# Kernel tuning notes

Hardware: AMD Instinct MI355X
Metric: run time of the kernel (lower is better)

The kernel has to match this reference:

```python
import jax, jax.numpy as jnp
import numpy as np

SIN, TEMB, EMB, S = 128, 512, 1024, 64
BATCH, T = 4, 4096


def setup_inputs() -> dict:
    key = jax.random.key(0)
    ks = jax.random.split(key, 16)

    def w(k, *shape):
        return jax.random.normal(k, shape, jnp.float32) / np.float32(np.sqrt(shape[0]))

    return {
        "time_embed": jax.random.normal(ks[0], (SIN,), jnp.float32),
        "x": jax.random.normal(ks[1], (BATCH, T, EMB), jnp.float32),
        "W1": w(ks[2], SIN, TEMB), "b1": jnp.zeros((TEMB,), jnp.float32),
        "W2": w(ks[3], TEMB, TEMB), "b2": jnp.zeros((TEMB,), jnp.float32),
        "WA": w(ks[4], TEMB, S), "bA": jnp.zeros((S,), jnp.float32),
        "WB": w(ks[5], TEMB, S, EMB), "bB": jnp.zeros((S, EMB), jnp.float32),
        "WC": w(ks[6], TEMB, EMB, S), "bC": jnp.zeros((EMB, S), jnp.float32),
        "WD": w(ks[7], TEMB, EMB), "bD": jnp.zeros((EMB,), jnp.float32),
        "Wdl": w(ks[8], TEMB, S), "bdl": jnp.zeros((S,), jnp.float32),
        "MA": w(ks[9], SIN, S), "mA": jnp.zeros((S,), jnp.float32),
        "MB": w(ks[10], SIN, S, EMB), "mB": jnp.zeros((S, EMB), jnp.float32),
        "MC": w(ks[11], SIN, EMB, S), "mC": jnp.zeros((EMB, S), jnp.float32),
        "MD": w(ks[12], SIN, EMB), "mD": jnp.zeros((EMB,), jnp.float32),
        "Mdl": w(ks[13], SIN, S), "mdl": jnp.zeros((S,), jnp.float32),
    }


def _ssm_forward(time_embed, x, W1, b1, W2, b2, WA, bA, WB, bB, WC, bC, WD, bD,
                 Wdl, bdl, MA, mA, MB, mB, MC, mC, MD, mD, Mdl, mdl):
    # time-dependent parameter generation
    t = jax.nn.silu(time_embed @ W1 + b1)
    t = t @ W2 + b2  # [TEMB]

    A_base = -jax.nn.softplus(t @ WA + bA)                       # [S]
    B_base = jnp.einsum('t,tse->se', t, WB) + bB                 # [S,E]
    C_base = jnp.einsum('t,tes->es', t, WC) + bC                 # [E,S]
    D_base = t @ WD + bD                                         # [E]
    delta_base = jax.nn.softplus(t @ Wdl + bdl) + 1e-4           # [S]

    A = A_base * jax.nn.sigmoid(time_embed @ MA + mA)
    Bm = B_base * jax.nn.sigmoid(jnp.einsum('t,tse->se', time_embed, MB) + mB)
    C = C_base * jax.nn.sigmoid(jnp.einsum('t,tes->es', time_embed, MC) + mC)
    D = D_base * jax.nn.sigmoid(time_embed @ MD + mD)
    delta = delta_base * jax.nn.sigmoid(time_embed @ Mdl + mdl)  # [S]

    A_bar = jnp.exp(delta * A)          # [S]
    B_bar = delta[:, None] * Bm         # [S,E]

    xt = jnp.swapaxes(x, 0, 1)          # [T,B,E]

    def step(h, x_t):                   # h: [B,S], x_t: [B,E]
        h_new = A_bar * h + x_t @ B_bar.T
        y = h_new @ C.T                 # [B,E]
        return h_new, y

    h0 = jnp.zeros((x.shape[0], A_bar.shape[0]), x.dtype)
    _, ys = jax.lax.scan(step, h0, xt)  # ys: [T,B,E]
    return jnp.swapaxes(ys, 0, 1) + D * x


def reference(time_embed, x, W1, b1, W2, b2, WA, bA, WB, bB, WC, bC, WD, bD,
              Wdl, bdl, MA, mA, MB, mB, MC, mC, MD, mD, Mdl, mdl):
    return _ssm_forward(time_embed, x, W1, b1, W2, b2, WA, bA, WB, bB, WC, bC,
                        WD, bD, Wdl, bdl, MA, mA, MB, mB, MC, mC, MD, mD, Mdl, mdl)
```

## Files before the change

kernel.cpp:

```cpp
#include <hip/hip_runtime.h>
#include <math.h>

#define SIN_ 128
#define TEMB_ 512
#define EMB_ 1024
#define S_ 64
#define B_ 4
#define T_ 4096
#define NROW (B_*T_)
#define L_ 32
#define NC_ (T_/L_)

#define GK 32
#define NSL 16
#define NCH 16
#define NGCH 4

#define WS_T1     0
#define WS_T2     512
#define WS_DELTA  1024
#define WS_ABAR   1088
#define WS_EL     1152
#define WS_FAC    1216
#define WS_D      3264
#define WS_BMT    4288
#define WS_CT     69824
#define WS_PD     135360
#define WS_PDG    151744
#define WS_PA     155840
#define WS_PDL    156160
#define WS_PBF    156480
#define WS_HLOC   156480
#define WS_CHEND  1205056
#define WS_CARRY  1237824

__device__ __forceinline__ float sigmoidf_(float x){ return 1.f/(1.f+expf(-x)); }
__device__ __forceinline__ float softplusf_(float x){ return x>20.f ? x : log1pf(expf(x)); }
__device__ __forceinline__ float4 sig4_(float4 g){
  float4 r; r.x=sigmoidf_(g.x); r.y=sigmoidf_(g.y); r.z=sigmoidf_(g.z); r.w=sigmoidf_(g.w); return r;
}
__device__ __forceinline__ unsigned short f2bf(float x){
  unsigned int u = __float_as_uint(x);
  unsigned int r = (u + 0x7FFFu + ((u>>16)&1u)) >> 16;
  return (unsigned short)r;
}
__device__ __forceinline__ ushort4 pack4(float4 v){
  return make_ushort4(f2bf(v.x),f2bf(v.y),f2bf(v.z),f2bf(v.w));
}
__device__ __forceinline__ float bf2f(unsigned short h){
  return __uint_as_float(((unsigned int)h)<<16);
}

__global__ void k_t1(const float* __restrict__ te, const float* __restrict__ W1,
                     const float* __restrict__ b1, float* __restrict__ ws){
  __shared__ float ste[SIN_];
  int tid = threadIdx.x;
  ste[tid] = te[tid]; ste[tid+64] = te[tid+64];
  __syncthreads();
  int j = blockIdx.x*64 + tid;
  float a = b1[j];
  #pragma unroll 16
  for (int i=0;i<SIN_;i++) a += ste[i]*W1[i*TEMB_ + j];
  ws[WS_T1 + j] = a * sigmoidf_(a);
}

__global__ __launch_bounds__(512) void k_t2(const float* __restrict__ W2,
                                            const float* __restrict__ b2,
                                            float* __restrict__ ws){
  __shared__ float st1[TEMB_];
  __shared__ float red[8][64];
  int tid = threadIdx.x;
  st1[tid] = ws[WS_T1 + tid];
  __syncthreads();
  int jl = tid & 63, kc = tid >> 6;
  int j = blockIdx.x*64 + jl;
  float p = 0.f;
  #pragma unroll 8
  for (int i=0;i<64;i++){
    int k = kc*64 + i;
    p += st1[k]*W2[k*TEMB_ + j];
  }
  red[kc][jl] = p;
  __syncthreads();
  if (tid < 64){
    float a = b2[blockIdx.x*64 + tid];
    #pragma unroll
    for (int c=0;c<8;c++) a += red[c][tid];
    ws[WS_T2 + blockIdx.x*64 + tid] = a;
  }
}

__global__ __launch_bounds__(256,2) void k_partial(
    const float* __restrict__ te,
    const float* __restrict__ WB, const float* __restrict__ MB,
    const float* __restrict__ WC, const float* __restrict__ MC,
    const float* __restrict__ WD, const float* __restrict__ MD,
    const float* __restrict__ WA, const float* __restrict__ MA,
    const float* __restrict__ Wdl, const float* __restrict__ Mdl,
    float* __restrict__ ws){
  __shared__ float st2[TEMB_];
  __shared__ float ste[SIN_];
  int tid = threadIdx.x;
  st2[tid] = ws[WS_T2 + tid];
  st2[tid+256] = ws[WS_T2 + tid + 256];
  if (tid < SIN_) ste[tid] = te[tid];
  __syncthreads();
  unsigned short* pbf = (unsigned short*)(ws + WS_PBF);
  int bb = blockIdx.x;
  if (bb < 512){
    int r = bb>>8, rem = bb&255, j = rem>>4, c = rem&15;
    const float4* W4 = (const float4*)(r ? WC : WB);
    const float4* base = W4 + (size_t)(c*GK)*16384 + j*1024 + tid;
    const float* coef = st2 + c*GK;
    float4 a0={0,0,0,0}, a1={0,0,0,0}, a2={0,0,0,0}, a3={0,0,0,0};
    #pragma unroll 4
    for (int k=0;k<GK;k++){
      const float4* p = base + (size_t)k*16384;
      float4 w0=p[0], w1=p[256], w2=p[512], w3=p[768];
      float cv = coef[k];
      a0.x=fmaf(cv,w0.x,a0.x); a0.y=fmaf(cv,w0.y,a0.y); a0.z=fmaf(cv,w0.z,a0.z); a0.w=fmaf(cv,w0.w,a0.w);
      a1.x=fmaf(cv,w1.x,a1.x); a1.y=fmaf(cv,w1.y,a1.y); a1.z=fmaf(cv,w1.z,a1.z); a1.w=fmaf(cv,w1.w,a1.w);
      a2.x=fmaf(cv,w2.x,a2.x); a2.y=fmaf(cv,w2.y,a2.y); a2.z=fmaf(cv,w2.z,a2.z); a2.w=fmaf(cv,w2.w,a2.w);
      a3.x=fmaf(cv,w3.x,a3.x); a3.y=fmaf(cv,w3.y,a3.y); a3.z=fmaf(cv,w3.z,a3.z); a3.w=fmaf(cv,w3.w,a3.w);
    }
    ushort4* dst = (ushort4*)pbf + (size_t)((r*NSL+j)*NCH + c)*1024;
    dst[tid]     = pack4(a0);
    dst[tid+256] = pack4(a1);
    dst[tid+512] = pack4(a2);
    dst[tid+768] = pack4(a3);
  } else if (bb < 640){
    int g = bb-512, r = g>>6, rem = g&63, j = rem>>2, cg = rem&3;
    const float4* M4 = (const float4*)(r ? MC : MB);
    const float4* base = M4 + (size_t)(cg*GK)*16384 + j*1024 + tid;
    const float* coef = ste + cg*GK;
    float4 a0={0,0,0,0}, a1={0,0,0,0}, a2={0,0,0,0}, a3={0,0,0,0};
    #pragma unroll 4
    for (int k=0;k<GK;k++){
      const float4* p = base + (size_t)k*16384;
      float4 w0=p[0], w1=p[256], w2=p[512], w3=p[768];
      float cv = coef[k];
      a0.x=fmaf(cv,w0.x,a0.x); a0.y=fmaf(cv,w0.y,a0.y); a0.z=fmaf(cv,w0.z,a0.z); a0.w=fmaf(cv,w0.w,a0.w);
      a1.x=fmaf(cv,w1.x,a1.x); a1.y=fmaf(cv,w1.y,a1.y); a1.z=fmaf(cv,w1.z,a1.z); a1.w=fmaf(cv,w1.w,a1.w);
      a2.x=fmaf(cv,w2.x,a2.x); a2.y=fmaf(cv,w2.y,a2.y); a2.z=fmaf(cv,w2.z,a2.z); a2.w=fmaf(cv,w2.w,a2.w);
      a3.x=fmaf(cv,w3.x,a3.x); a3.y=fmaf(cv,w3.y,a3.y); a3.z=fmaf(cv,w3.z,a3.z); a3.w=fmaf(cv,w3.w,a3.w);
    }
    ushort4* dst = (ushort4*)pbf + (size_t)(2097152/4) + (size_t)((r*NSL+j)*NGCH + cg)*1024;
    dst[tid]     = pack4(a0);
    dst[tid+256] = pack4(a1);
    dst[tid+512] = pack4(a2);
    dst[tid+768] = pack4(a3);
  } else if (bb < 656){
    int c = bb-640;
    const float4* base = (const float4*)WD + (size_t)(c*GK)*256 + tid;
    const float* coef = st2 + c*GK;
    float4 a={0,0,0,0};
    #pragma unroll 4
    for (int k=0;k<GK;k++){
      float4 w = base[(size_t)k*256];
      float cv = coef[k];
      a.x=fmaf(cv,w.x,a.x); a.y=fmaf(cv,w.y,a.y); a.z=fmaf(cv,w.z,a.z); a.w=fmaf(cv,w.w,a.w);
    }
    ((float4*)(ws + WS_PD))[c*256 + tid] = a;
  } else if (bb < 660){
    int cg = bb-656;
    const float4* base = (const float4*)MD + (size_t)(cg*GK)*256 + tid;
    const float* coef = ste + cg*GK;
    float4 a={0,0,0,0};
    #pragma unroll 4
    for (int k=0;k<GK;k++){
      float4 w = base[(size_t)k*256];
      float cv = coef[k];
      a.x=fmaf(cv,w.x,a.x); a.y=fmaf(cv,w.y,a.y); a.z=fmaf(cv,w.z,a.z); a.w=fmaf(cv,w.w,a.w);
    }
    ((float4*)(ws + WS_PDG))[cg*256 + tid] = a;
  } else {
    const float* Wm = (bb==660) ? WA : Wdl;
    const float* Mm = (bb==660) ? MA : Mdl;
    int outbase = (bb==660) ? WS_PA : WS_PDL;
    __shared__ float red[16][68];
    int q = tid&15, kr = tid>>4;
    float4 acc={0,0,0,0};
    const float4* W4 = (const float4*)Wm;
    #pragma unroll 4
    for (int it=0; it<32; ++it){
      int k = it*16 + kr;
      float4 w = W4[k*16 + q];
      float cv = st2[k];
      acc.x=fmaf(cv,w.x,acc.x); acc.y=fmaf(cv,w.y,acc.y); acc.z=fmaf(cv,w.z,acc.z); acc.w=fmaf(cv,w.w,acc.w);
    }
    red[kr][4*q+0]=acc.x; red[kr][4*q+1]=acc.y; red[kr][4*q+2]=acc.z; red[kr][4*q+3]=acc.w;
    __syncthreads();
    if (tid < 64){
      float s = 0.f;
      #pragma unroll
      for (int g=0;g<16;g++) s += red[g][tid];
      ws[outbase + tid] = s;
    }
    __syncthreads();
    float4 gac={0,0,0,0};
    const float4* M4 = (const float4*)Mm;
    #pragma unroll 4
    for (int it=0; it<8; ++it){
      int k = it*16 + kr;
      float4 w = M4[k*16 + q];
      float cv = ste[k];
      gac.x=fmaf(cv,w.x,gac.x); gac.y=fmaf(cv,w.y,gac.y); gac.z=fmaf(cv,w.z,gac.z); gac.w=fmaf(cv,w.w,gac.w);
    }
    red[kr][4*q+0]=gac.x; red[kr][4*q+1]=gac.y; red[kr][4*q+2]=gac.z; red[kr][4*q+3]=gac.w;
    __syncthreads();
    if (tid < 64){
      float s = 0.f;
      #pragma unroll
      for (int g=0;g<16;g++) s += red[g][tid];
      ws[outbase + 64 + tid] = s;
    }
  }
}

__global__ __launch_bounds__(256) void k_finalize(
    const float* __restrict__ bB, const float* __restrict__ mB,
    const float* __restrict__ bC, const float* __restrict__ mC,
    const float* __restrict__ bD, const float* __restrict__ mD,
    const float* __restrict__ bA_, const float* __restrict__ mA_,
    const float* __restrict__ bdl, const float* __restrict__ mdl,
    float* __restrict__ ws){
  int tid = threadIdx.x, bb = blockIdx.x;
  const ushort4* pbf4 = (const ushort4*)(ws + WS_PBF);
  if (bb < 128){
    int r = bb>>6;
    int q = (bb&63)*256 + tid;
    int j = q>>10, p = q&1023;
    float4 a = {0,0,0,0};
    size_t wbase = (size_t)((r*NSL+j)*NCH)*1024 + p;
    #pragma unroll
    for (int c=0;c<NCH;c++){
      ushort4 v = pbf4[wbase + (size_t)c*1024];
      a.x += bf2f(v.x); a.y += bf2f(v.y); a.z += bf2f(v.z); a.w += bf2f(v.w);
    }
    float4 g = {0,0,0,0};
    size_t gbase = (size_t)(2097152/4) + (size_t)((r*NSL+j)*NGCH)*1024 + p;
    #pragma unroll
    for (int cg=0;cg<NGCH;cg++){
      ushort4 v = pbf4[gbase + (size_t)cg*1024];
      g.x += bf2f(v.x); g.y += bf2f(v.y); g.z += bf2f(v.z); g.w += bf2f(v.w);
    }
    if (r == 0){
      float4 b4 = ((const float4*)bB)[q];
      float4 m4 = ((const float4*)mB)[q];
      float4 sg = sig4_(make_float4(g.x+m4.x, g.y+m4.y, g.z+m4.z, g.w+m4.w));
      float4 v = make_float4((a.x+b4.x)*sg.x,(a.y+b4.y)*sg.y,(a.z+b4.z)*sg.z,(a.w+b4.w)*sg.w);
      int o = q*4; int s = o>>10; int e = o&1023;
      ws[WS_BMT + (e+0)*64 + s] = v.x;
      ws[WS_BMT + (e+1)*64 + s] = v.y;
      ws[WS_BMT + (e+2)*64 + s] = v.z;
      ws[WS_BMT + (e+3)*64 + s] = v.w;
    } else {
      float4 b4 = ((const float4*)bC)[q];
      float4 m4 = ((const float4*)mC)[q];
      float4 sg = sig4_(make_float4(g.x+m4.x, g.y+m4.y, g.z+m4.z, g.w+m4.w));
      float4 v = make_float4((a.x+b4.x)*sg.x,(a.y+b4.y)*sg.y,(a.z+b4.z)*sg.z,(a.w+b4.w)*sg.w);
      int o = q*4; int e = o>>6; int s = o&63;
      ws[WS_CT + (s+0)*1024 + e] = v.x;
      ws[WS_CT + (s+1)*1024 + e] = v.y;
      ws[WS_CT + (s+2)*1024 + e] = v.z;
      ws[WS_CT + (s+3)*1024 + e] = v.w;
    }
  } else if (bb == 128){
    float4 a = {0,0,0,0};
    #pragma unroll
    for (int c=0;c<NCH;c++){
      float4 v = ((const float4*)(ws + WS_PD))[c*256 + tid];
      a.x+=v.x; a.y+=v.y; a.z+=v.z; a.w+=v.w;
    }
    float4 g = {0,0,0,0};
    #pragma unroll
    for (int cg=0;cg<NGCH;cg++){
      float4 v = ((const float4*)(ws + WS_PDG))[cg*256 + tid];
      g.x+=v.x; g.y+=v.y; g.z+=v.z; g.w+=v.w;
    }
    float4 b4 = ((const float4*)bD)[tid];
    float4 m4 = ((const float4*)mD)[tid];
    float4 sg = sig4_(make_float4(g.x+m4.x, g.y+m4.y, g.z+m4.z, g.w+m4.w));
    float4 v = make_float4((a.x+b4.x)*sg.x,(a.y+b4.y)*sg.y,(a.z+b4.z)*sg.z,(a.w+b4.w)*sg.w);
    ((float4*)(ws + WS_D))[tid] = v;
  } else {
    __shared__ float sda[64];
    if (tid < 64){
      int s = tid;
      float A = -softplusf_(ws[WS_PA+s] + bA_[s]) * sigmoidf_(ws[WS_PA+64+s] + mA_[s]);
      float delta = (softplusf_(ws[WS_PDL+s] + bdl[s]) + 1e-4f) * sigmoidf_(ws[WS_PDL+64+s] + mdl[s]);
      float da = delta * A;
      sda[s] = da;
      ws[WS_DELTA+s] = delta;
      ws[WS_ABAR+s]  = expf(da);
      ws[WS_EL+s]    = expf((float)L_*da);
    }
    __syncthreads();
    for (int idx=tid; idx<L_*S_; idx+=256){
      int tl = idx>>6, s = idx&63;
      ws[WS_FAC+idx] = expf((float)(tl+1)*sda[s]);
    }
  }
}

__global__ __launch_bounds__(256) void k_scan(const float* __restrict__ x, float* __restrict__ ws){
  __shared__ float Xs[32][68];
  __shared__ float BsT[64][68];
  __shared__ float Us[32][65];
  __shared__ float sdl[S_], sab[S_];
  int tid = threadIdx.x;
  int bb = blockIdx.x;
  int row0 = (bb>>7)*T_ + (bb&127)*L_;
  if (tid<64){ sdl[tid]=ws[WS_DELTA+tid]; sab[tid]=ws[WS_ABAR+tid]; }
  float acc[2][4];
  #pragma unroll
  for (int i=0;i<2;i++)
    #pragma unroll
    for (int j=0;j<4;j++) acc[i][j]=0.f;
  int ty = tid>>4, tx = tid&15;
  const float4* x4 = (const float4*)x;
  const float4* BmT4 = (const float4*)(ws + WS_BMT);
  for (int kk=0; kk<EMB_; kk+=64){
    #pragma unroll
    for (int t=0;t<2;t++){
      int fl = t*256+tid; int rr = fl>>4, cq = fl&15;
      float4 xv = x4[(size_t)(row0+rr)*256 + (kk>>2) + cq];
      *(float4*)&Xs[rr][cq*4] = xv;
    }
    #pragma unroll
    for (int t=0;t<4;t++){
      int fl = t*256+tid; int rr = fl>>4, cq = fl&15;
      float4 bv = BmT4[(size_t)(kk+rr)*16 + cq];
      *(float4*)&BsT[rr][cq*4] = bv;
    }
    __syncthreads();
    #pragma unroll 8
    for (int k=0;k<64;k++){
      float4 b4 = *(const float4*)&BsT[k][4*tx];
      float x0 = Xs[2*ty+0][k], x1 = Xs[2*ty+1][k];
      acc[0][0]+=x0*b4.x; acc[0][1]+=x0*b4.y; acc[0][2]+=x0*b4.z; acc[0][3]+=x0*b4.w;
      acc[1][0]+=x1*b4.x; acc[1][1]+=x1*b4.y; acc[1][2]+=x1*b4.z; acc[1][3]+=x1*b4.w;
    }
    __syncthreads();
  }
  #pragma unroll
  for (int i=0;i<2;i++)
    #pragma unroll
    for (int j=0;j<4;j++)
      Us[2*ty+i][4*tx+j] = acc[i][j]*sdl[4*tx+j];
  __syncthreads();
  if (tid<64){
    int s = tid; float h = 0.f, ab = sab[s];
    #pragma unroll 8
    for (int t=0;t<L_;t++){
      h = fmaf(ab, h, Us[t][s]);
      ws[WS_HLOC + (row0+t)*S_ + s] = h;
    }
    ws[WS_CHEND + bb*S_ + s] = h;
  }
}

__global__ void k_carry(float* __restrict__ ws){
  int tid = threadIdx.x;
  int b = tid>>6, s = tid&63;
  float el = ws[WS_EL + s];
  float carry = 0.f;
  #pragma unroll 8
  for (int c=0;c<NC_;c++){
    int idx = (b*NC_ + c)*S_ + s;
    ws[WS_CARRY + idx] = carry;
    carry = fmaf(el, carry, ws[WS_CHEND + idx]);
  }
}

__global__ __launch_bounds__(256) void k_out(const float* __restrict__ x,
                                             const float* __restrict__ ws,
                                             float* __restrict__ out){
  __shared__ float Cts[64][68];
  __shared__ float Hs[64][68];
  int tid = threadIdx.x;
  int bb = blockIdx.x;
  int rt = bb & 255, et = bb >> 8;
  int row0 = rt*64, e0 = et*64;
  int b = row0 >> 12;
  int cbase = b*NC_ + ((row0 & (T_-1)) >> 5);
  const float4* hl4 = (const float4*)(ws + WS_HLOC);
  const float4* fc4 = (const float4*)(ws + WS_FAC);
  const float4* cr4 = (const float4*)(ws + WS_CARRY);
  const float4* CT4 = (const float4*)(ws + WS_CT);
  #pragma unroll
  for (int t=0;t<4;t++){
    int fl = t*256+tid; int rr = fl>>4, q = fl&15;
    float4 h = hl4[(size_t)(row0+rr)*16 + q];
    float4 f = fc4[(rr & (L_-1))*16 + q];
    float4 c = cr4[(cbase + (rr>>5))*16 + q];
    float4 hv = make_float4(h.x+f.x*c.x, h.y+f.y*c.y, h.z+f.z*c.z, h.w+f.w*c.w);
    *(float4*)&Hs[rr][q*4] = hv;
    float4 ct = CT4[(size_t)rr*256 + (e0>>2) + q];
    *(float4*)&Cts[rr][q*4] = ct;
  }
  __syncthreads();
  int ty = tid>>4, tx = tid&15;
  float acc[4][4];
  #pragma unroll
  for (int i=0;i<4;i++)
    #pragma unroll
    for (int j=0;j<4;j++) acc[i][j]=0.f;
  #pragma unroll 8
  for (int s=0;s<64;s++){
    float4 c4 = *(const float4*)&Cts[s][4*tx];
    float h0 = Hs[4*ty+0][s], h1 = Hs[4*ty+1][s], h2 = Hs[4*ty+2][s], h3 = Hs[4*ty+3][s];
    acc[0][0]+=h0*c4.x; acc[0][1]+=h0*c4.y; acc[0][2]+=h0*c4.z; acc[0][3]+=h0*c4.w;
    acc[1][0]+=h1*c4.x; acc[1][1]+=h1*c4.y; acc[1][2]+=h1*c4.z; acc[1][3]+=h1*c4.w;
    acc[2][0]+=h2*c4.x; acc[2][1]+=h2*c4.y; acc[2][2]+=h2*c4.z; acc[2][3]+=h2*c4.w;
    acc[3][0]+=h3*c4.x; acc[3][1]+=h3*c4.y; acc[3][2]+=h3*c4.z; acc[3][3]+=h3*c4.w;
  }
  float4 d4 = ((const float4*)(ws + WS_D))[(e0>>2) + tx];
  #pragma unroll
  for (int i=0;i<4;i++){
    int row = row0 + 4*ty + i;
    float4 x4v = reinterpret_cast<const float4*>(x + (size_t)row*EMB_ + e0)[tx];
    float4 o;
    o.x = acc[i][0] + d4.x*x4v.x;
    o.y = acc[i][1] + d4.y*x4v.y;
    o.z = acc[i][2] + d4.z*x4v.z;
    o.w = acc[i][3] + d4.w*x4v.w;
    reinterpret_cast<float4*>(out + (size_t)row*EMB_ + e0)[tx] = o;
  }
}

extern "C" void kernel_launch(void* const* d_in, const int* in_sizes, int n_in,
                              void* d_out, int out_size, void* d_ws, size_t ws_size,
                              hipStream_t stream){
  const float* te  = (const float*)d_in[0];
  const float* x   = (const float*)d_in[1];
  const float* W1  = (const float*)d_in[2];
  const float* b1  = (const float*)d_in[3];
  const float* W2  = (const float*)d_in[4];
  const float* b2  = (const float*)d_in[5];
  const float* WA  = (const float*)d_in[6];
  const float* bA  = (const float*)d_in[7];
  const float* WB  = (const float*)d_in[8];
  const float* bB  = (const float*)d_in[9];
  const float* WC  = (const float*)d_in[10];
  const float* bC  = (const float*)d_in[11];
  const float* WD  = (const float*)d_in[12];
  const float* bD  = (const float*)d_in[13];
  const float* Wdl = (const float*)d_in[14];
  const float* bdl = (const float*)d_in[15];
  const float* MA  = (const float*)d_in[16];
  const float* mA  = (const float*)d_in[17];
  const float* MB  = (const float*)d_in[18];
  const float* mB  = (const float*)d_in[19];
  const float* MC  = (const float*)d_in[20];
  const float* mC  = (const float*)d_in[21];
  const float* MD  = (const float*)d_in[22];
  const float* mD  = (const float*)d_in[23];
  const float* Mdl = (const float*)d_in[24];
  const float* mdl = (const float*)d_in[25];
  float* ws  = (float*)d_ws;
  float* out = (float*)d_out;

  k_t1<<<8,64,0,stream>>>(te, W1, b1, ws);
  k_t2<<<8,512,0,stream>>>(W2, b2, ws);
  k_partial<<<662,256,0,stream>>>(te, WB,MB, WC,MC, WD,MD, WA,MA, Wdl,Mdl, ws);
  k_finalize<<<130,256,0,stream>>>(bB,mB, bC,mC, bD,mD, bA,mA, bdl,mdl, ws);
  k_scan<<<512,256,0,stream>>>(x, ws);
  k_carry<<<1,256,0,stream>>>(ws);
  k_out<<<4096,256,0,stream>>>(x, ws, out);
}
```

Baseline: 192.0 us.

## Stream weight-generation GEMV through LDS ring with async global_load_lds

The large B/C weight reduction in k_partial now prefetches each row slice into a 4-deep LDS ring using direct global-to-LDS loads, with vmcnt waits and barriers. Each block handles half the columns it did before (NSL doubled), so the grid roughly doubles, and k_finalize indexing is updated to match. The goal is more memory-level parallelism and better latency hiding on this bandwidth-bound weight read. The cost is extra barriers per iteration and dropping the two-blocks-per-CU launch bound.

```diff
diff --git a/kernel.cpp b/kernel.cpp
--- a/kernel.cpp
+++ b/kernel.cpp
@@ -12,7 +12,7 @@
 #define NC_ (T_/L_)
 
 #define GK 32
-#define NSL 16
+#define NSL 32
 #define NCH 16
 #define NGCH 4
 
@@ -50,6 +50,11 @@
 __device__ __forceinline__ float bf2f(unsigned short h){
   return __uint_as_float(((unsigned int)h)<<16);
 }
+__device__ __forceinline__ void gll16(const void* g, void* l){
+  __builtin_amdgcn_global_load_lds((const __attribute__((address_space(1))) void*)g,
+                                   (__attribute__((address_space(3))) void*)l, 16, 0, 0);
+}
+#define WAITV(N) asm volatile("s_waitcnt vmcnt(" #N ")" ::: "memory")
 
 __global__ void k_t1(const float* __restrict__ te, const float* __restrict__ W1,
                      const float* __restrict__ b1, float* __restrict__ ws){
@@ -90,7 +95,7 @@
   }
 }
 
-__global__ __launch_bounds__(256,2) void k_partial(
+__global__ __launch_bounds__(256) void k_partial(
     const float* __restrict__ te,
     const float* __restrict__ WB, const float* __restrict__ MB,
     const float* __restrict__ WC, const float* __restrict__ MC,
@@ -98,6 +103,7 @@
     const float* __restrict__ WA, const float* __restrict__ MA,
     const float* __restrict__ Wdl, const float* __restrict__ Mdl,
     float* __restrict__ ws){
+  __shared__ float ring[4][2048];
   __shared__ float st2[TEMB_];
   __shared__ float ste[SIN_];
   int tid = threadIdx.x;
@@ -106,51 +112,54 @@
   if (tid < SIN_) ste[tid] = te[tid];
   __syncthreads();
   unsigned short* pbf = (unsigned short*)(ws + WS_PBF);
+  ushort4* pbf4 = (ushort4*)pbf;
   int bb = blockIdx.x;
-  if (bb < 512){
-    int r = bb>>8, rem = bb&255, j = rem>>4, c = rem&15;
-    const float4* W4 = (const float4*)(r ? WC : WB);
-    const float4* base = W4 + (size_t)(c*GK)*16384 + j*1024 + tid;
-    const float* coef = st2 + c*GK;
-    float4 a0={0,0,0,0}, a1={0,0,0,0}, a2={0,0,0,0}, a3={0,0,0,0};
-    #pragma unroll 4
+  if (bb < 1280){
+    const float4* W4; const float* coef; size_t row0; ushort4* dst;
+    int j;
+    if (bb < 1024){
+      int r = bb>>9, rem = bb&511, c = rem&15; j = rem>>4;
+      W4 = (const float4*)(r ? WC : WB);
+      coef = st2 + c*GK; row0 = (size_t)c*GK;
+      dst = pbf4 + ((size_t)(r*NSL+j)*NCH + c)*512;
+    } else {
+      int g = bb-1024, r = g>>7, rem = g&127, cg = rem&3; j = rem>>2;
+      W4 = (const float4*)(r ? MC : MB);
+      coef = ste + cg*GK; row0 = (size_t)cg*GK;
+      dst = pbf4 + 524288 + ((size_t)(r*NSL+j)*NGCH + cg)*512;
+    }
+    int w = tid>>6, lane = tid&63;
+    char* rbase = (char*)&ring[0][0];
+    const int j512 = j*512;
+    auto stage = [&](int row, int slot){
+      const float4* gp = W4 + (row0 + row)*16384 + j512 + (w*128 + lane);
+      char* lp = rbase + slot*8192 + w*2048;
+      gll16(gp,      lp);
+      gll16(gp + 64, lp + 1024);
+    };
+    #pragma unroll
+    for (int p0=0;p0<4;p0++) stage(p0, p0);
+    float4 a0={0,0,0,0}, a1={0,0,0,0};
     for (int k=0;k<GK;k++){
-      const float4* p = base + (size_t)k*16384;
-      float4 w0=p[0], w1=p[256], w2=p[512], w3=p[768];
+      int slot = k & 3;
+      int rem = GK-1-k;
+      if (rem>=3) WAITV(6); else if (rem==2) WAITV(4); else if (rem==1) WAITV(2); else WAITV(0);
+      __builtin_amdgcn_s_barrier();
+      asm volatile("" ::: "memory");
+      const char* rb = rbase + slot*8192;
+      float4 w0 = *(const float4*)(rb + tid*16);
+      float4 w1 = *(const float4*)(rb + 4096 + tid*16);
       float cv = coef[k];
       a0.x=fmaf(cv,w0.x,a0.x); a0.y=fmaf(cv,w0.y,a0.y); a0.z=fmaf(cv,w0.z,a0.z); a0.w=fmaf(cv,w0.w,a0.w);
       a1.x=fmaf(cv,w1.x,a1.x); a1.y=fmaf(cv,w1.y,a1.y); a1.z=fmaf(cv,w1.z,a1.z); a1.w=fmaf(cv,w1.w,a1.w);
-      a2.x=fmaf(cv,w2.x,a2.x); a2.y=fmaf(cv,w2.y,a2.y); a2.z=fmaf(cv,w2.z,a2.z); a2.w=fmaf(cv,w2.w,a2.w);
-      a3.x=fmaf(cv,w3.x,a3.x); a3.y=fmaf(cv,w3.y,a3.y); a3.z=fmaf(cv,w3.z,a3.z); a3.w=fmaf(cv,w3.w,a3.w);
-    }
-    ushort4* dst = (ushort4*)pbf + (size_t)((r*NSL+j)*NCH + c)*1024;
+      asm volatile("s_waitcnt lgkmcnt(0)" ::: "memory");
+      __builtin_amdgcn_s_barrier();
+      if (k+4 < GK) stage(k+4, slot);
+    }
     dst[tid]     = pack4(a0);
     dst[tid+256] = pack4(a1);
-    dst[tid+512] = pack4(a2);
-    dst[tid+768] = pack4(a3);
-  } else if (bb < 640){
-    int g = bb-512, r = g>>6, rem = g&63, j = rem>>2, cg = rem&3;
-    const float4* M4 = (const float4*)(r ? MC : MB);
-    const float4* base = M4 + (size_t)(cg*GK)*16384 + j*1024 + tid;
-    const float* coef = ste + cg*GK;
-    float4 a0={0,0,0,0}, a1={0,0,0,0}, a2={0,0,0,0}, a3={0,0,0,0};
-    #pragma unroll 4
-    for (int k=0;k<GK;k++){
-      const float4* p = base + (size_t)k*16384;
-      float4 w0=p[0], w1=p[256], w2=p[512], w3=p[768];
-      float cv = coef[k];
-      a0.x=fmaf(cv,w0.x,a0.x); a0.y=fmaf(cv,w0.y,a0.y); a0.z=fmaf(cv,w0.z,a0.z); a0.w=fmaf(cv,w0.w,a0.w);
-      a1.x=fmaf(cv,w1.x,a1.x); a1.y=fmaf(cv,w1.y,a1.y); a1.z=fmaf(cv,w1.z,a1.z); a1.w=fmaf(cv,w1.w,a1.w);
-      a2.x=fmaf(cv,w2.x,a2.x); a2.y=fmaf(cv,w2.y,a2.y); a2.z=fmaf(cv,w2.z,a2.z); a2.w=fmaf(cv,w2.w,a2.w);
-      a3.x=fmaf(cv,w3.x,a3.x); a3.y=fmaf(cv,w3.y,a3.y); a3.z=fmaf(cv,w3.z,a3.z); a3.w=fmaf(cv,w3.w,a3.w);
-    }
-    ushort4* dst = (ushort4*)pbf + (size_t)(2097152/4) + (size_t)((r*NSL+j)*NGCH + cg)*1024;
-    dst[tid]     = pack4(a0);
-    dst[tid+256] = pack4(a1);
-    dst[tid+512] = pack4(a2);
-    dst[tid+768] = pack4(a3);
-  } else if (bb < 656){
-    int c = bb-640;
+  } else if (bb < 1296){
+    int c = bb-1280;
     const float4* base = (const float4*)WD + (size_t)(c*GK)*256 + tid;
     const float* coef = st2 + c*GK;
     float4 a={0,0,0,0};
@@ -161,8 +170,8 @@
       a.x=fmaf(cv,w.x,a.x); a.y=fmaf(cv,w.y,a.y); a.z=fmaf(cv,w.z,a.z); a.w=fmaf(cv,w.w,a.w);
     }
     ((float4*)(ws + WS_PD))[c*256 + tid] = a;
-  } else if (bb < 660){
-    int cg = bb-656;
+  } else if (bb < 1300){
+    int cg = bb-1296;
     const float4* base = (const float4*)MD + (size_t)(cg*GK)*256 + tid;
     const float* coef = ste + cg*GK;
     float4 a={0,0,0,0};
@@ -174,9 +183,9 @@
     }
     ((float4*)(ws + WS_PDG))[cg*256 + tid] = a;
   } else {
-    const float* Wm = (bb==660) ? WA : Wdl;
-    const float* Mm = (bb==660) ? MA : Mdl;
-    int outbase = (bb==660) ? WS_PA : WS_PDL;
+    const float* Wm = (bb==1300) ? WA : Wdl;
+    const float* Mm = (bb==1300) ? MA : Mdl;
+    int outbase = (bb==1300) ? WS_PA : WS_PDL;
     __shared__ float red[16][68];
     int q = tid&15, kr = tid>>4;
     float4 acc={0,0,0,0};
@@ -229,19 +238,19 @@
   if (bb < 128){
     int r = bb>>6;
     int q = (bb&63)*256 + tid;
-    int j = q>>10, p = q&1023;
+    int j = q>>9, p = q&511;
     float4 a = {0,0,0,0};
-    size_t wbase = (size_t)((r*NSL+j)*NCH)*1024 + p;
+    size_t wbase = ((size_t)(r*NSL+j)*NCH)*512 + p;
     #pragma unroll
     for (int c=0;c<NCH;c++){
-      ushort4 v = pbf4[wbase + (size_t)c*1024];
+      ushort4 v = pbf4[wbase + (size_t)c*512];
       a.x += bf2f(v.x); a.y += bf2f(v.y); a.z += bf2f(v.z); a.w += bf2f(v.w);
     }
     float4 g = {0,0,0,0};
-    size_t gbase = (size_t)(2097152/4) + (size_t)((r*NSL+j)*NGCH)*1024 + p;
+    size_t gbase = 524288 + ((size_t)(r*NSL+j)*NGCH)*512 + p;
     #pragma unroll
     for (int cg=0;cg<NGCH;cg++){
-      ushort4 v = pbf4[gbase + (size_t)cg*1024];
+      ushort4 v = pbf4[gbase + (size_t)cg*512];
       g.x += bf2f(v.x); g.y += bf2f(v.y); g.z += bf2f(v.z); g.w += bf2f(v.w);
     }
     if (r == 0){
@@ -463,7 +472,7 @@
 
   k_t1<<<8,64,0,stream>>>(te, W1, b1, ws);
   k_t2<<<8,512,0,stream>>>(W2, b2, ws);
-  k_partial<<<662,256,0,stream>>>(te, WB,MB, WC,MC, WD,MD, WA,MA, Wdl,Mdl, ws);
+  k_partial<<<1302,256,0,stream>>>(te, WB,MB, WC,MC, WD,MD, WA,MA, Wdl,Mdl, ws);
   k_finalize<<<130,256,0,stream>>>(bB,mB, bC,mC, bD,mD, bA,mA, bdl,mdl, ws);
   k_scan<<<512,256,0,stream>>>(x, ws);
   k_carry<<<1,256,0,stream>>>(ws);
```

Result: no change. 193.6 us (+0.8%).

## Store B, C and local scan states in bf16; stage carry scan through LDS

Applied to the files above, without the earlier changes.

The transposed B and C matrices and the per-row local hidden states are now written to the workspace as bf16 and widened to fp32 on load in the scan and output kernels, which halves that intermediate traffic. The carry kernel copies the chunk-end states into shared memory, runs its serial scan there, and writes the carries back with vectorised stores, instead of making strided global round trips inside the loop. Rounding B, C and the hidden states to bf16 lowers accuracy.

```diff
diff --git a/kernel.cpp b/kernel.cpp
--- a/kernel.cpp
+++ b/kernel.cpp
@@ -23,16 +23,16 @@
 #define WS_EL     1152
 #define WS_FAC    1216
 #define WS_D      3264
-#define WS_BMT    4288
-#define WS_CT     69824
-#define WS_PD     135360
-#define WS_PDG    151744
-#define WS_PA     155840
-#define WS_PDL    156160
-#define WS_PBF    156480
-#define WS_HLOC   156480
-#define WS_CHEND  1205056
-#define WS_CARRY  1237824
+#define WS_BMTH   4288
+#define WS_CTH    37056
+#define WS_PD     69824
+#define WS_PDG    86208
+#define WS_PA     90304
+#define WS_PDL    90432
+#define WS_PBF    90560
+#define WS_HLOCH  90560
+#define WS_CHEND  1401280
+#define WS_CARRY  1434048
 
 __device__ __forceinline__ float sigmoidf_(float x){ return 1.f/(1.f+expf(-x)); }
 __device__ __forceinline__ float softplusf_(float x){ return x>20.f ? x : log1pf(expf(x)); }
@@ -144,7 +144,7 @@
       a2.x=fmaf(cv,w2.x,a2.x); a2.y=fmaf(cv,w2.y,a2.y); a2.z=fmaf(cv,w2.z,a2.z); a2.w=fmaf(cv,w2.w,a2.w);
       a3.x=fmaf(cv,w3.x,a3.x); a3.y=fmaf(cv,w3.y,a3.y); a3.z=fmaf(cv,w3.z,a3.z); a3.w=fmaf(cv,w3.w,a3.w);
     }
-    ushort4* dst = (ushort4*)pbf + (size_t)(2097152/4) + (size_t)((r*NSL+j)*NGCH + cg)*1024;
+    ushort4* dst = (ushort4*)pbf + (size_t)524288 + (size_t)((r*NSL+j)*NGCH + cg)*1024;
     dst[tid]     = pack4(a0);
     dst[tid+256] = pack4(a1);
     dst[tid+512] = pack4(a2);
@@ -226,19 +226,21 @@
     float* __restrict__ ws){
   int tid = threadIdx.x, bb = blockIdx.x;
   const ushort4* pbf4 = (const ushort4*)(ws + WS_PBF);
+  unsigned short* bmth = (unsigned short*)(ws + WS_BMTH);
+  unsigned short* cth  = (unsigned short*)(ws + WS_CTH);
   if (bb < 128){
     int r = bb>>6;
     int q = (bb&63)*256 + tid;
     int j = q>>10, p = q&1023;
     float4 a = {0,0,0,0};
-    size_t wbase = (size_t)((r*NSL+j)*NCH)*1024 + p;
+    size_t wbase = ((size_t)(r*NSL+j)*NCH)*1024 + p;
     #pragma unroll
     for (int c=0;c<NCH;c++){
       ushort4 v = pbf4[wbase + (size_t)c*1024];
       a.x += bf2f(v.x); a.y += bf2f(v.y); a.z += bf2f(v.z); a.w += bf2f(v.w);
     }
     float4 g = {0,0,0,0};
-    size_t gbase = (size_t)(2097152/4) + (size_t)((r*NSL+j)*NGCH)*1024 + p;
+    size_t gbase = (size_t)524288 + ((size_t)(r*NSL+j)*NGCH)*1024 + p;
     #pragma unroll
     for (int cg=0;cg<NGCH;cg++){
       ushort4 v = pbf4[gbase + (size_t)cg*1024];
@@ -250,20 +252,20 @@
       float4 sg = sig4_(make_float4(g.x+m4.x, g.y+m4.y, g.z+m4.z, g.w+m4.w));
       float4 v = make_float4((a.x+b4.x)*sg.x,(a.y+b4.y)*sg.y,(a.z+b4.z)*sg.z,(a.w+b4.w)*sg.w);
       int o = q*4; int s = o>>10; int e = o&1023;
-      ws[WS_BMT + (e+0)*64 + s] = v.x;
-      ws[WS_BMT + (e+1)*64 + s] = v.y;
-      ws[WS_BMT + (e+2)*64 + s] = v.z;
-      ws[WS_BMT + (e+3)*64 + s] = v.w;
+      bmth[(e+0)*64 + s] = f2bf(v.x);
+      bmth[(e+1)*64 + s] = f2bf(v.y);
+      bmth[(e+2)*64 + s] = f2bf(v.z);
+      bmth[(e+3)*64 + s] = f2bf(v.w);
     } else {
       float4 b4 = ((const float4*)bC)[q];
       float4 m4 = ((const float4*)mC)[q];
       float4 sg = sig4_(make_float4(g.x+m4.x, g.y+m4.y, g.z+m4.z, g.w+m4.w));
       float4 v = make_float4((a.x+b4.x)*sg.x,(a.y+b4.y)*sg.y,(a.z+b4.z)*sg.z,(a.w+b4.w)*sg.w);
       int o = q*4; int e = o>>6; int s = o&63;
-      ws[WS_CT + (s+0)*1024 + e] = v.x;
-      ws[WS_CT + (s+1)*1024 + e] = v.y;
-      ws[WS_CT + (s+2)*1024 + e] = v.z;
-      ws[WS_CT + (s+3)*1024 + e] = v.w;
+      cth[(s+0)*1024 + e] = f2bf(v.x);
+      cth[(s+1)*1024 + e] = f2bf(v.y);
+      cth[(s+2)*1024 + e] = f2bf(v.z);
+      cth[(s+3)*1024 + e] = f2bf(v.w);
     }
   } else if (bb == 128){
     float4 a = {0,0,0,0};
@@ -319,7 +321,7 @@
     for (int j=0;j<4;j++) acc[i][j]=0.f;
   int ty = tid>>4, tx = tid&15;
   const float4* x4 = (const float4*)x;
-  const float4* BmT4 = (const float4*)(ws + WS_BMT);
+  const ushort4* bm4 = (const ushort4*)(ws + WS_BMTH);
   for (int kk=0; kk<EMB_; kk+=64){
     #pragma unroll
     for (int t=0;t<2;t++){
@@ -330,8 +332,8 @@
     #pragma unroll
     for (int t=0;t<4;t++){
       int fl = t*256+tid; int rr = fl>>4, cq = fl&15;
-      float4 bv = BmT4[(size_t)(kk+rr)*16 + cq];
-      *(float4*)&BsT[rr][cq*4] = bv;
+      ushort4 hv = bm4[(size_t)(kk+rr)*16 + cq];
+      *(float4*)&BsT[rr][cq*4] = make_float4(bf2f(hv.x),bf2f(hv.y),bf2f(hv.z),bf2f(hv.w));
     }
     __syncthreads();
     #pragma unroll 8
@@ -350,27 +352,37 @@
       Us[2*ty+i][4*tx+j] = acc[i][j]*sdl[4*tx+j];
   __syncthreads();
   if (tid<64){
+    unsigned short* hh = (unsigned short*)(ws + WS_HLOCH);
     int s = tid; float h = 0.f, ab = sab[s];
     #pragma unroll 8
     for (int t=0;t<L_;t++){
       h = fmaf(ab, h, Us[t][s]);
-      ws[WS_HLOC + (row0+t)*S_ + s] = h;
+      hh[(size_t)(row0+t)*S_ + s] = f2bf(h);
     }
     ws[WS_CHEND + bb*S_ + s] = h;
   }
 }
 
-__global__ void k_carry(float* __restrict__ ws){
-  int tid = threadIdx.x;
+__global__ __launch_bounds__(256) void k_carry(float* __restrict__ ws){
+  __shared__ float ch[B_*NC_*S_];
+  int tid = threadIdx.x;
+  const float4* src = (const float4*)(ws + WS_CHEND);
+  float4* chv = (float4*)ch;
+  for (int i=tid;i<8192;i+=256) chv[i] = src[i];
+  __syncthreads();
   int b = tid>>6, s = tid&63;
   float el = ws[WS_EL + s];
   float carry = 0.f;
   #pragma unroll 8
   for (int c=0;c<NC_;c++){
     int idx = (b*NC_ + c)*S_ + s;
-    ws[WS_CARRY + idx] = carry;
-    carry = fmaf(el, carry, ws[WS_CHEND + idx]);
-  }
+    float v = ch[idx];
+    ch[idx] = carry;
+    carry = fmaf(el, carry, v);
+  }
+  __syncthreads();
+  float4* dst = (float4*)(ws + WS_CARRY);
+  for (int i=tid;i<8192;i+=256) dst[i] = chv[i];
 }
 
 __global__ __launch_bounds__(256) void k_out(const float* __restrict__ x,
@@ -384,20 +396,21 @@
   int row0 = rt*64, e0 = et*64;
   int b = row0 >> 12;
   int cbase = b*NC_ + ((row0 & (T_-1)) >> 5);
-  const float4* hl4 = (const float4*)(ws + WS_HLOC);
+  const ushort4* hl4h = (const ushort4*)(ws + WS_HLOCH);
+  const ushort4* cth4 = (const ushort4*)(ws + WS_CTH);
   const float4* fc4 = (const float4*)(ws + WS_FAC);
   const float4* cr4 = (const float4*)(ws + WS_CARRY);
-  const float4* CT4 = (const float4*)(ws + WS_CT);
   #pragma unroll
   for (int t=0;t<4;t++){
     int fl = t*256+tid; int rr = fl>>4, q = fl&15;
-    float4 h = hl4[(size_t)(row0+rr)*16 + q];
+    ushort4 h4 = hl4h[(size_t)(row0+rr)*16 + q];
     float4 f = fc4[(rr & (L_-1))*16 + q];
     float4 c = cr4[(cbase + (rr>>5))*16 + q];
-    float4 hv = make_float4(h.x+f.x*c.x, h.y+f.y*c.y, h.z+f.z*c.z, h.w+f.w*c.w);
+    float4 hv = make_float4(bf2f(h4.x)+f.x*c.x, bf2f(h4.y)+f.y*c.y,
+                            bf2f(h4.z)+f.z*c.z, bf2f(h4.w)+f.w*c.w);
     *(float4*)&Hs[rr][q*4] = hv;
-    float4 ct = CT4[(size_t)rr*256 + (e0>>2) + q];
-    *(float4*)&Cts[rr][q*4] = ct;
+    ushort4 ct4 = cth4[(size_t)rr*256 + (e0>>2) + q];
+    *(float4*)&Cts[rr][q*4] = make_float4(bf2f(ct4.x),bf2f(ct4.y),bf2f(ct4.z),bf2f(ct4.w));
   }
   __syncthreads();
   int ty = tid>>4, tx = tid&15;
```

Result: faster. 187.0 us (-2.6%).
